# Optimization experiments

Measured on AMD Instinct MI355X. Metric: run time of the kernel, lower is better.

## Reference

```python
import jax, jax.numpy as jnp
import numpy as np

NUM_HEADS = 8


def setup_inputs() -> dict:
    key = jax.random.key(0)
    ks = jax.random.split(key, 10)
    B, C, H, W = 8, 256, 128, 128
    x_c = jax.random.normal(ks[0], (B, C, H, W), dtype=jnp.float32)
    x_t = jax.random.normal(ks[1], (B, C, H, W), dtype=jnp.float32)
    std = 0.02
    Wq = jax.random.normal(ks[2], (C, C), dtype=jnp.float32) * std
    Wk = jax.random.normal(ks[3], (C, C), dtype=jnp.float32) * std
    Wv = jax.random.normal(ks[4], (C, C), dtype=jnp.float32) * std
    Wo = jax.random.normal(ks[5], (C, C), dtype=jnp.float32) * std
    bq = jnp.zeros((C,), jnp.float32)
    bk = jnp.zeros((C,), jnp.float32)
    bv = jnp.zeros((C,), jnp.float32)
    bo = jnp.zeros((C,), jnp.float32)
    return {"x_c": x_c, "x_t": x_t, "Wq": Wq, "bq": bq, "Wk": Wk, "bk": bk,
            "Wv": Wv, "bv": bv, "Wo": Wo, "bo": bo}


def reference(x_c, x_t, Wq, bq, Wk, bk, Wv, bv, Wo, bo):
    B, C, H, W = x_c.shape
    nh = NUM_HEADS
    hd = C // nh                       # head_dim = in_chans // num_heads
    scale = hd ** (-0.5)
    N = H * W

    # fuse_type == 'add'
    x = (x_c + x_t).transpose(0, 2, 3, 1)          # [B,H,W,C]

    # torch Linear: y = x @ W.T + b
    q = x @ Wq.T + bq
    k = x @ Wk.T + bk
    v = x @ Wv.T + bv

    # 'b h w (c head) -> b (h w) head c' : head is the INNER split factor
    def split_heads(t):
        return t.reshape(B, N, hd, nh).transpose(0, 1, 3, 2)  # [B,N,nh,hd]

    q, k, v = split_heads(q), split_heads(k), split_heads(v)

    # attention ACROSS heads per token: [B,N,nh,nh] (faithful to source)
    dot = jnp.einsum('bnhc,bngc->bnhg', q, k) * scale
    attn = jax.nn.softmax(dot, axis=-1)
    o = jnp.einsum('bnhg,bngc->bnhc', attn, v)     # [B,N,nh,hd]

    # 'b (h w) head c -> b h w (head c)' : head is the OUTER concat factor
    o = o.reshape(B, H, W, nh * hd)
    out = o @ Wo.T + bo                            # [B,H,W,C]
    return out.transpose(0, 3, 1, 2)               # [B,C,H,W]
```

## Files before the change

### kernel.cpp

```cpp
#include <hip/hip_runtime.h>
#include <hip/hip_bf16.h>


typedef unsigned short u16;
typedef __bf16 bf16x8 __attribute__((ext_vector_type(8)));
typedef float f32x4 __attribute__((ext_vector_type(4)));
typedef unsigned short u16x8 __attribute__((ext_vector_type(8)));
typedef unsigned short u16x4 __attribute__((ext_vector_type(4)));

constexpr int CH = 256;
constexpr int HWN = 16384;
constexpr int T = 32;
constexpr int LDXe = 272;
constexpr int LDOe = 280;
constexpr int LQe  = 776;

constexpr size_t WS_WQKV = 0;
constexpr size_t WS_WO   = 393216;
constexpr size_t WS_BIAS = 524288;

__device__ __forceinline__ u16 f2bf(float f) {
    unsigned u = __builtin_bit_cast(unsigned, f);
    unsigned r = u + 0x7FFFu + ((u >> 16) & 1u);
    return (u16)(r >> 16);
}
__device__ __forceinline__ float bf2f(u16 u) {
    return __builtin_bit_cast(float, (unsigned)u << 16);
}

__global__ void prep_kernel(const float* __restrict__ Wq, const float* __restrict__ Wk,
                            const float* __restrict__ Wv, const float* __restrict__ Wo,
                            const float* __restrict__ bq, const float* __restrict__ bk,
                            const float* __restrict__ bv,
                            u16* __restrict__ Wqkv_b, u16* __restrict__ Wo_b,
                            float* __restrict__ bias_qkv) {
    const int i = blockIdx.x;
    const int c = threadIdx.x;
    const int j = i & 255;
    const int p = ((j & 31) << 3) + (j >> 5);
    const float* Wsrc = (i < 256) ? Wq : (i < 512 ? Wk : Wv);
    const float* bsrc = (i < 256) ? bq : (i < 512 ? bk : bv);
    Wqkv_b[i * 256 + c] = f2bf(Wsrc[p * 256 + c]);
    if (i < 256) Wo_b[i * 256 + c] = f2bf(Wo[i * 256 + c]);
    if (c == 0) bias_qkv[i] = bsrc[p];
}

__launch_bounds__(512, 4)
__global__ void fused_kernel(const float* __restrict__ x_c, const float* __restrict__ x_t,
                             const u16* __restrict__ Wqkv_b, const u16* __restrict__ Wo_b,
                             const float* __restrict__ bias_qkv, const float* __restrict__ bo,
                             float* __restrict__ out) {
    __shared__ u16 XO[T * LDOe];
    __shared__ u16 QKVT[T * LQe];

    const int tid = threadIdx.x;
    const int lane = tid & 63;
    const int wave = tid >> 6;
    const int tok0 = blockIdx.x * T;
    const int b = tok0 >> 14;
    const int hw0 = tok0 & (HWN - 1);
    const float* __restrict__ xc = x_c + (size_t)b * CH * HWN + hw0;
    const float* __restrict__ xt = x_t + (size_t)b * CH * HWN + hw0;

    {
        const int t2 = (tid & 15) * 2;
        const int c0 = (tid >> 4) * 8;
        float2 va[8], vb[8];
#pragma unroll
        for (int j = 0; j < 8; ++j) {
            const size_t off = (size_t)(c0 + j) * HWN + t2;
            va[j] = *(const float2*)&xc[off];
            vb[j] = *(const float2*)&xt[off];
        }
        u16x8 r0, r1;
#pragma unroll
        for (int j = 0; j < 8; ++j) {
            r0[j] = f2bf(va[j].x + vb[j].x);
            r1[j] = f2bf(va[j].y + vb[j].y);
        }
        *(u16x8*)&XO[t2 * LDXe + c0] = r0;
        *(u16x8*)&XO[(t2 + 1) * LDXe + c0] = r1;
    }
    __syncthreads();

    {
        const int l15 = lane & 15;
        const int l4 = lane >> 4;
        const int m_base = wave * 96;
        f32x4 acc[6][2];
#pragma unroll
        for (int i = 0; i < 6; ++i)
#pragma unroll
            for (int j = 0; j < 2; ++j) acc[i][j] = (f32x4){0.f, 0.f, 0.f, 0.f};

#pragma unroll
        for (int kk = 0; kk < 8; ++kk) {
            const int koff = kk * 32 + l4 * 8;
            bf16x8 bfr[2];
#pragma unroll
            for (int ct = 0; ct < 2; ++ct)
                bfr[ct] = __builtin_bit_cast(bf16x8,
                    *(const u16x8*)&XO[(ct * 16 + l15) * LDXe + koff]);
#pragma unroll
            for (int mt = 0; mt < 6; ++mt) {
                const bf16x8 afr = __builtin_bit_cast(bf16x8,
                    *(const u16x8*)&Wqkv_b[(m_base + mt * 16 + l15) * 256 + koff]);
#pragma unroll
                for (int ct = 0; ct < 2; ++ct)
                    acc[mt][ct] = __builtin_amdgcn_mfma_f32_16x16x32_bf16(
                        afr, bfr[ct], acc[mt][ct], 0, 0, 0);
            }
        }
#pragma unroll
        for (int mt = 0; mt < 6; ++mt) {
            const int i0 = m_base + mt * 16 + l4 * 4;
            const f32x4 bias = *(const f32x4*)&bias_qkv[i0];
#pragma unroll
            for (int ct = 0; ct < 2; ++ct) {
                const int t = ct * 16 + l15;
                u16x4 pk;
#pragma unroll
                for (int r = 0; r < 4; ++r) pk[r] = f2bf(acc[mt][ct][r] + bias[r]);
                *(u16x4*)&QKVT[t * LQe + i0] = pk;
            }
        }
    }
    __syncthreads();

    if (tid < T * 8) {
        const int t = tid >> 3;
        const int h = tid & 7;
        const u16* __restrict__ row = &QKVT[t * LQe];
        float q[32];
#pragma unroll
        for (int i = 0; i < 4; ++i) {
            const u16x8 v = *(const u16x8*)&row[h * 32 + i * 8];
#pragma unroll
            for (int e = 0; e < 8; ++e) q[i * 8 + e] = bf2f(v[e]);
        }
        float dot[8];
#pragma unroll
        for (int g = 0; g < 8; ++g) {
            float s = 0.f;
#pragma unroll
            for (int i = 0; i < 4; ++i) {
                const u16x8 v = *(const u16x8*)&row[256 + g * 32 + i * 8];
#pragma unroll
                for (int e = 0; e < 8; ++e) s += q[i * 8 + e] * bf2f(v[e]);
            }
            dot[g] = s * 0.17677669529663687f;
        }
        float m = dot[0];
#pragma unroll
        for (int g = 1; g < 8; ++g) m = fmaxf(m, dot[g]);
        float ssum = 0.f;
#pragma unroll
        for (int g = 0; g < 8; ++g) { dot[g] = __expf(dot[g] - m); ssum += dot[g]; }
        const float rinv = 1.f / ssum;
        float o[32];
#pragma unroll
        for (int i = 0; i < 32; ++i) o[i] = 0.f;
#pragma unroll
        for (int g = 0; g < 8; ++g) {
            const float w = dot[g] * rinv;
#pragma unroll
            for (int i = 0; i < 4; ++i) {
                const u16x8 v = *(const u16x8*)&row[512 + g * 32 + i * 8];
#pragma unroll
                for (int e = 0; e < 8; ++e) o[i * 8 + e] += w * bf2f(v[e]);
            }
        }
#pragma unroll
        for (int i = 0; i < 4; ++i) {
            u16x8 pk;
#pragma unroll
            for (int e = 0; e < 8; ++e) pk[e] = f2bf(o[i * 8 + e]);
            *(u16x8*)&XO[t * LDOe + h * 32 + i * 8] = pk;
        }
    }
    __syncthreads();

    {
        const int l15 = lane & 15;
        const int l4 = lane >> 4;
        const int m_base = wave * 32;
        f32x4 acc[2][2];
#pragma unroll
        for (int i = 0; i < 2; ++i)
#pragma unroll
            for (int j = 0; j < 2; ++j) acc[i][j] = (f32x4){0.f, 0.f, 0.f, 0.f};

#pragma unroll
        for (int kk = 0; kk < 8; ++kk) {
            const int koff = kk * 32 + l4 * 8;
            bf16x8 bfr[2];
#pragma unroll
            for (int ct = 0; ct < 2; ++ct)
                bfr[ct] = __builtin_bit_cast(bf16x8,
                    *(const u16x8*)&XO[(ct * 16 + l15) * LDOe + koff]);
#pragma unroll
            for (int mt = 0; mt < 2; ++mt) {
                const bf16x8 afr = __builtin_bit_cast(bf16x8,
                    *(const u16x8*)&Wo_b[(m_base + mt * 16 + l15) * 256 + koff]);
#pragma unroll
                for (int ct = 0; ct < 2; ++ct)
                    acc[mt][ct] = __builtin_amdgcn_mfma_f32_16x16x32_bf16(
                        afr, bfr[ct], acc[mt][ct], 0, 0, 0);
            }
        }
#pragma unroll
        for (int mt = 0; mt < 2; ++mt) {
            const int c0 = m_base + mt * 16 + l4 * 4;
            const f32x4 bias = *(const f32x4*)&bo[c0];
#pragma unroll
            for (int ct = 0; ct < 2; ++ct) {
                const int hw = hw0 + ct * 16 + l15;
                float* __restrict__ op = out + (((size_t)b * 256 + c0) << 14) + hw;
#pragma unroll
                for (int r = 0; r < 4; ++r)
                    op[(size_t)r << 14] = acc[mt][ct][r] + bias[r];
            }
        }
    }
}

extern "C" void kernel_launch(void* const* d_in, const int* in_sizes, int n_in,
                              void* d_out, int out_size, void* d_ws, size_t ws_size,
                              hipStream_t stream) {
    const float* x_c = (const float*)d_in[0];
    const float* x_t = (const float*)d_in[1];
    const float* Wq = (const float*)d_in[2];
    const float* bq = (const float*)d_in[3];
    const float* Wk = (const float*)d_in[4];
    const float* bk = (const float*)d_in[5];
    const float* Wv = (const float*)d_in[6];
    const float* bv = (const float*)d_in[7];
    const float* Wo = (const float*)d_in[8];
    const float* bo = (const float*)d_in[9];
    float* out = (float*)d_out;
    char* ws = (char*)d_ws;

    u16* Wqkv_b = (u16*)(ws + WS_WQKV);
    u16* Wo_b = (u16*)(ws + WS_WO);
    float* bias_qkv = (float*)(ws + WS_BIAS);

    prep_kernel<<<768, 256, 0, stream>>>(Wq, Wk, Wv, Wo, bq, bk, bv,
                                         Wqkv_b, Wo_b, bias_qkv);
    fused_kernel<<<(8 * HWN) / T, 512, 0, stream>>>(x_c, x_t, Wqkv_b, Wo_b,
                                                    bias_qkv, bo, out);
}
```

Measured before the change: 600.7 us.

## Make fused kernel persistent with input prefetch and LDS-staged coalesced output stores

Launches 512 persistent blocks that loop over token tiles, prefetching the next tile's x_c/x_t into registers while the current tile runs its QKV GEMM, attention and output GEMM. Output is staged through LDS per wave so each channel row is written as contiguous float4 stores instead of scattered scalar stores. The XO buffer is merged into a single XT buffer with a smaller pad, and the attention output accumulation is restructured to use fewer live registers. The risks are lower parallelism from only 512 blocks, higher register pressure from holding the prefetched inputs, and LDS bank conflicts from the new padding.

```diff
diff --git a/kernel.cpp b/kernel.cpp
--- a/kernel.cpp
+++ b/kernel.cpp
@@ -11,9 +11,10 @@
 constexpr int CH = 256;
 constexpr int HWN = 16384;
 constexpr int T = 32;
-constexpr int LDXe = 272;
-constexpr int LDOe = 280;
+constexpr int LDXe = 264;
 constexpr int LQe  = 776;
+constexpr int NBLK = 512;
+constexpr int NITER = (8 * HWN / T) / NBLK;
 
 constexpr size_t WS_WQKV = 0;
 constexpr size_t WS_WO   = 393216;
@@ -50,177 +51,203 @@
                              const u16* __restrict__ Wqkv_b, const u16* __restrict__ Wo_b,
                              const float* __restrict__ bias_qkv, const float* __restrict__ bo,
                              float* __restrict__ out) {
-    __shared__ u16 XO[T * LDOe];
+    __shared__ u16 XT[T * LDXe];
     __shared__ u16 QKVT[T * LQe];
 
     const int tid = threadIdx.x;
     const int lane = tid & 63;
     const int wave = tid >> 6;
-    const int tok0 = blockIdx.x * T;
-    const int b = tok0 >> 14;
-    const int hw0 = tok0 & (HWN - 1);
-    const float* __restrict__ xc = x_c + (size_t)b * CH * HWN + hw0;
-    const float* __restrict__ xt = x_t + (size_t)b * CH * HWN + hw0;
+    const int l15 = lane & 15;
+    const int l4 = lane >> 4;
+
+    const int t2 = (tid & 15) * 2;
+    const int cg = (tid >> 4) * 8;
+
+    float2 va[8], vb[8];
 
     {
-        const int t2 = (tid & 15) * 2;
-        const int c0 = (tid >> 4) * 8;
-        float2 va[8], vb[8];
+        const int tok0 = blockIdx.x * T;
+        const size_t base = (size_t)(tok0 >> 14) * CH * HWN + (tok0 & (HWN - 1)) + t2;
+        const float* pc = x_c + base + (size_t)cg * HWN;
+        const float* pt = x_t + base + (size_t)cg * HWN;
 #pragma unroll
         for (int j = 0; j < 8; ++j) {
-            const size_t off = (size_t)(c0 + j) * HWN + t2;
-            va[j] = *(const float2*)&xc[off];
-            vb[j] = *(const float2*)&xt[off];
-        }
-        u16x8 r0, r1;
-#pragma unroll
-        for (int j = 0; j < 8; ++j) {
-            r0[j] = f2bf(va[j].x + vb[j].x);
-            r1[j] = f2bf(va[j].y + vb[j].y);
-        }
-        *(u16x8*)&XO[t2 * LDXe + c0] = r0;
-        *(u16x8*)&XO[(t2 + 1) * LDXe + c0] = r1;
+            va[j] = *(const float2*)&pc[(size_t)j * HWN];
+            vb[j] = *(const float2*)&pt[(size_t)j * HWN];
+        }
     }
-    __syncthreads();
-
-    {
-        const int l15 = lane & 15;
-        const int l4 = lane >> 4;
-        const int m_base = wave * 96;
-        f32x4 acc[6][2];
-#pragma unroll
-        for (int i = 0; i < 6; ++i)
-#pragma unroll
-            for (int j = 0; j < 2; ++j) acc[i][j] = (f32x4){0.f, 0.f, 0.f, 0.f};
-
-#pragma unroll
-        for (int kk = 0; kk < 8; ++kk) {
-            const int koff = kk * 32 + l4 * 8;
-            bf16x8 bfr[2];
-#pragma unroll
-            for (int ct = 0; ct < 2; ++ct)
-                bfr[ct] = __builtin_bit_cast(bf16x8,
-                    *(const u16x8*)&XO[(ct * 16 + l15) * LDXe + koff]);
+
+    for (int it = 0; it < NITER; ++it) {
+        const int tile = it * NBLK + blockIdx.x;
+        const int tok0 = tile * T;
+        const int b = tok0 >> 14;
+        const int hw0 = tok0 & (HWN - 1);
+
+        {
+            u16x8 r0, r1;
+#pragma unroll
+            for (int j = 0; j < 8; ++j) {
+                r0[j] = f2bf(va[j].x + vb[j].x);
+                r1[j] = f2bf(va[j].y + vb[j].y);
+            }
+            *(u16x8*)&XT[t2 * LDXe + cg] = r0;
+            *(u16x8*)&XT[(t2 + 1) * LDXe + cg] = r1;
+        }
+        __syncthreads();
+
+        if (it + 1 < NITER) {
+            const int ntok0 = (tile + NBLK) * T;
+            const size_t base = (size_t)(ntok0 >> 14) * CH * HWN + (ntok0 & (HWN - 1)) + t2;
+            const float* pc = x_c + base + (size_t)cg * HWN;
+            const float* pt = x_t + base + (size_t)cg * HWN;
+#pragma unroll
+            for (int j = 0; j < 8; ++j) {
+                va[j] = *(const float2*)&pc[(size_t)j * HWN];
+                vb[j] = *(const float2*)&pt[(size_t)j * HWN];
+            }
+        }
+        {
+            const int m_base = wave * 96;
+            f32x4 acc[6][2];
+#pragma unroll
+            for (int i = 0; i < 6; ++i)
+#pragma unroll
+                for (int j = 0; j < 2; ++j) acc[i][j] = (f32x4){0.f, 0.f, 0.f, 0.f};
+
+#pragma unroll
+            for (int kk = 0; kk < 8; ++kk) {
+                const int koff = kk * 32 + l4 * 8;
+                bf16x8 bfr[2];
+#pragma unroll
+                for (int ct = 0; ct < 2; ++ct)
+                    bfr[ct] = __builtin_bit_cast(bf16x8,
+                        *(const u16x8*)&XT[(ct * 16 + l15) * LDXe + koff]);
+#pragma unroll
+                for (int mt = 0; mt < 6; ++mt) {
+                    const bf16x8 afr = __builtin_bit_cast(bf16x8,
+                        *(const u16x8*)&Wqkv_b[(m_base + mt * 16 + l15) * 256 + koff]);
+#pragma unroll
+                    for (int ct = 0; ct < 2; ++ct)
+                        acc[mt][ct] = __builtin_amdgcn_mfma_f32_16x16x32_bf16(
+                            afr, bfr[ct], acc[mt][ct], 0, 0, 0);
+                }
+            }
 #pragma unroll
             for (int mt = 0; mt < 6; ++mt) {
-                const bf16x8 afr = __builtin_bit_cast(bf16x8,
-                    *(const u16x8*)&Wqkv_b[(m_base + mt * 16 + l15) * 256 + koff]);
+                const int i0 = m_base + mt * 16 + l4 * 4;
+                const f32x4 bias = *(const f32x4*)&bias_qkv[i0];
+#pragma unroll
+                for (int ct = 0; ct < 2; ++ct) {
+                    const int t = ct * 16 + l15;
+                    u16x4 pk;
+#pragma unroll
+                    for (int r = 0; r < 4; ++r) pk[r] = f2bf(acc[mt][ct][r] + bias[r]);
+                    *(u16x4*)&QKVT[t * LQe + i0] = pk;
+                }
+            }
+        }
+        __syncthreads();
+
+        if (tid < T * 8) {
+            const int t = tid >> 3;
+            const int h = tid & 7;
+            const u16* __restrict__ row = &QKVT[t * LQe];
+            float q[32];
+#pragma unroll
+            for (int i = 0; i < 4; ++i) {
+                const u16x8 v = *(const u16x8*)&row[h * 32 + i * 8];
+#pragma unroll
+                for (int e = 0; e < 8; ++e) q[i * 8 + e] = bf2f(v[e]);
+            }
+            float w8[8];
+#pragma unroll
+            for (int g = 0; g < 8; ++g) {
+                float s = 0.f;
+#pragma unroll
+                for (int i = 0; i < 4; ++i) {
+                    const u16x8 v = *(const u16x8*)&row[256 + g * 32 + i * 8];
+#pragma unroll
+                    for (int e = 0; e < 8; ++e) s += q[i * 8 + e] * bf2f(v[e]);
+                }
+                w8[g] = s * 0.17677669529663687f;
+            }
+            float m = w8[0];
+#pragma unroll
+            for (int g = 1; g < 8; ++g) m = fmaxf(m, w8[g]);
+            float ssum = 0.f;
+#pragma unroll
+            for (int g = 0; g < 8; ++g) { w8[g] = __expf(w8[g] - m); ssum += w8[g]; }
+            const float rinv = 1.f / ssum;
+#pragma unroll
+            for (int g = 0; g < 8; ++g) w8[g] *= rinv;
+#pragma unroll
+            for (int i = 0; i < 4; ++i) {
+                float o8[8];
+#pragma unroll
+                for (int e = 0; e < 8; ++e) o8[e] = 0.f;
+#pragma unroll
+                for (int g = 0; g < 8; ++g) {
+                    const u16x8 v = *(const u16x8*)&row[512 + g * 32 + i * 8];
+#pragma unroll
+                    for (int e = 0; e < 8; ++e) o8[e] += w8[g] * bf2f(v[e]);
+                }
+                u16x8 pk;
+#pragma unroll
+                for (int e = 0; e < 8; ++e) pk[e] = f2bf(o8[e]);
+                *(u16x8*)&XT[t * LDXe + h * 32 + i * 8] = pk;
+            }
+        }
+        __syncthreads();
+
+        {
+            const int m_base = wave * 32;
+            f32x4 acc[2][2];
+#pragma unroll
+            for (int i = 0; i < 2; ++i)
+#pragma unroll
+                for (int j = 0; j < 2; ++j) acc[i][j] = (f32x4){0.f, 0.f, 0.f, 0.f};
+
+#pragma unroll
+            for (int kk = 0; kk < 8; ++kk) {
+                const int koff = kk * 32 + l4 * 8;
+                bf16x8 bfr[2];
 #pragma unroll
                 for (int ct = 0; ct < 2; ++ct)
-                    acc[mt][ct] = __builtin_amdgcn_mfma_f32_16x16x32_bf16(
-                        afr, bfr[ct], acc[mt][ct], 0, 0, 0);
-            }
-        }
-#pragma unroll
-        for (int mt = 0; mt < 6; ++mt) {
-            const int i0 = m_base + mt * 16 + l4 * 4;
-            const f32x4 bias = *(const f32x4*)&bias_qkv[i0];
-#pragma unroll
-            for (int ct = 0; ct < 2; ++ct) {
-                const int t = ct * 16 + l15;
-                u16x4 pk;
-#pragma unroll
-                for (int r = 0; r < 4; ++r) pk[r] = f2bf(acc[mt][ct][r] + bias[r]);
-                *(u16x4*)&QKVT[t * LQe + i0] = pk;
-            }
-        }
-    }
-    __syncthreads();
-
-    if (tid < T * 8) {
-        const int t = tid >> 3;
-        const int h = tid & 7;
-        const u16* __restrict__ row = &QKVT[t * LQe];
-        float q[32];
-#pragma unroll
-        for (int i = 0; i < 4; ++i) {
-            const u16x8 v = *(const u16x8*)&row[h * 32 + i * 8];
-#pragma unroll
-            for (int e = 0; e < 8; ++e) q[i * 8 + e] = bf2f(v[e]);
-        }
-        float dot[8];
-#pragma unroll
-        for (int g = 0; g < 8; ++g) {
-            float s = 0.f;
-#pragma unroll
-            for (int i = 0; i < 4; ++i) {
-                const u16x8 v = *(const u16x8*)&row[256 + g * 32 + i * 8];
-#pragma unroll
-                for (int e = 0; e < 8; ++e) s += q[i * 8 + e] * bf2f(v[e]);
-            }
-            dot[g] = s * 0.17677669529663687f;
-        }
-        float m = dot[0];
-#pragma unroll
-        for (int g = 1; g < 8; ++g) m = fmaxf(m, dot[g]);
-        float ssum = 0.f;
-#pragma unroll
-        for (int g = 0; g < 8; ++g) { dot[g] = __expf(dot[g] - m); ssum += dot[g]; }
-        const float rinv = 1.f / ssum;
-        float o[32];
-#pragma unroll
-        for (int i = 0; i < 32; ++i) o[i] = 0.f;
-#pragma unroll
-        for (int g = 0; g < 8; ++g) {
-            const float w = dot[g] * rinv;
-#pragma unroll
-            for (int i = 0; i < 4; ++i) {
-                const u16x8 v = *(const u16x8*)&row[512 + g * 32 + i * 8];
-#pragma unroll
-                for (int e = 0; e < 8; ++e) o[i * 8 + e] += w * bf2f(v[e]);
-            }
-        }
-#pragma unroll
-        for (int i = 0; i < 4; ++i) {
-            u16x8 pk;
-#pragma unroll
-            for (int e = 0; e < 8; ++e) pk[e] = f2bf(o[i * 8 + e]);
-            *(u16x8*)&XO[t * LDOe + h * 32 + i * 8] = pk;
-        }
-    }
-    __syncthreads();
-
-    {
-        const int l15 = lane & 15;
-        const int l4 = lane >> 4;
-        const int m_base = wave * 32;
-        f32x4 acc[2][2];
-#pragma unroll
-        for (int i = 0; i < 2; ++i)
-#pragma unroll
-            for (int j = 0; j < 2; ++j) acc[i][j] = (f32x4){0.f, 0.f, 0.f, 0.f};
-
-#pragma unroll
-        for (int kk = 0; kk < 8; ++kk) {
-            const int koff = kk * 32 + l4 * 8;
-            bf16x8 bfr[2];
-#pragma unroll
-            for (int ct = 0; ct < 2; ++ct)
-                bfr[ct] = __builtin_bit_cast(bf16x8,
-                    *(const u16x8*)&XO[(ct * 16 + l15) * LDOe + koff]);
+                    bfr[ct] = __builtin_bit_cast(bf16x8,
+                        *(const u16x8*)&XT[(ct * 16 + l15) * LDXe + koff]);
+#pragma unroll
+                for (int mt = 0; mt < 2; ++mt) {
+                    const bf16x8 afr = __builtin_bit_cast(bf16x8,
+                        *(const u16x8*)&Wo_b[(m_base + mt * 16 + l15) * 256 + koff]);
+#pragma unroll
+                    for (int ct = 0; ct < 2; ++ct)
+                        acc[mt][ct] = __builtin_amdgcn_mfma_f32_16x16x32_bf16(
+                            afr, bfr[ct], acc[mt][ct], 0, 0, 0);
+                }
+            }
+            float* __restrict__ sw = (float*)QKVT + wave * 1152;
+            const size_t outbase = ((size_t)b * CH) << 14;
 #pragma unroll
             for (int mt = 0; mt < 2; ++mt) {
-                const bf16x8 afr = __builtin_bit_cast(bf16x8,
-                    *(const u16x8*)&Wo_b[(m_base + mt * 16 + l15) * 256 + koff]);
+                float* __restrict__ swm = sw + mt * 576;
 #pragma unroll
                 for (int ct = 0; ct < 2; ++ct)
-                    acc[mt][ct] = __builtin_amdgcn_mfma_f32_16x16x32_bf16(
-                        afr, bfr[ct], acc[mt][ct], 0, 0, 0);
-            }
-        }
-#pragma unroll
-        for (int mt = 0; mt < 2; ++mt) {
-            const int c0 = m_base + mt * 16 + l4 * 4;
-            const f32x4 bias = *(const f32x4*)&bo[c0];
-#pragma unroll
-            for (int ct = 0; ct < 2; ++ct) {
-                const int hw = hw0 + ct * 16 + l15;
-                float* __restrict__ op = out + (((size_t)b * 256 + c0) << 14) + hw;
-#pragma unroll
-                for (int r = 0; r < 4; ++r)
-                    op[(size_t)r << 14] = acc[mt][ct][r] + bias[r];
-            }
-        }
+#pragma unroll
+                    for (int r = 0; r < 4; ++r)
+                        swm[(l4 * 4 + r) * 36 + ct * 16 + l15] = acc[mt][ct][r];
+                asm volatile("s_waitcnt lgkmcnt(0)" ::: "memory");
+#pragma unroll
+                for (int j = 0; j < 2; ++j) {
+                    const int ch = (lane >> 3) + 8 * j;
+                    const int c0 = m_base + mt * 16 + ch;
+                    f32x4 v = *(const f32x4*)&swm[ch * 36 + (lane & 7) * 4];
+                    const float bb = bo[c0];
+                    v[0] += bb; v[1] += bb; v[2] += bb; v[3] += bb;
+                    *(f32x4*)&out[outbase + ((size_t)c0 << 14) + hw0 + (lane & 7) * 4] = v;
+                }
+            }
+        }
+        __syncthreads();
     }
 }
 
@@ -246,6 +273,6 @@
 
     prep_kernel<<<768, 256, 0, stream>>>(Wq, Wk, Wv, Wo, bq, bk, bv,
                                          Wqkv_b, Wo_b, bias_qkv);
-    fused_kernel<<<(8 * HWN) / T, 512, 0, stream>>>(x_c, x_t, Wqkv_b, Wo_b,
-                                                    bias_qkv, bo, out);
-}
+    fused_kernel<<<NBLK, 512, 0, stream>>>(x_c, x_t, Wqkv_b, Wo_b,
+                                           bias_qkv, bo, out);
+}
```

Measured after the change: 980.3 us. +63.2%, slower.
